# Optimization experiments

Hardware: AMD Instinct MI355X
Metric: run time of the kernel (lower is better)

## Reference

```python
import jax, jax.numpy as jnp
import numpy as np

B, SQ, SK, HID, H, D = 2, 2048, 2048, 1024, 16, 64
LN_EPS = 1e-12


def _sinusoid(seq_len):
    # [1,1,S,D]: first half sin, second half cos (RoFormer convention)
    pos = np.arange(seq_len, dtype=np.float32)[:, None]
    inv_freq = 1.0 / (10000.0 ** (np.arange(0, D, 2, dtype=np.float32) / D))
    ang = pos * inv_freq  # [S, D/2]
    return jnp.asarray(np.concatenate([np.sin(ang), np.cos(ang)], axis=-1)[None, None], dtype=jnp.float32)


def setup_inputs() -> dict:
    key = jax.random.key(0)
    ks = jax.random.split(key, 12)
    w = lambda k, shape: jax.random.normal(k, shape, dtype=jnp.float32) * 0.02
    return {
        "hidden_states": jax.random.normal(ks[0], (B, SQ, HID), dtype=jnp.float32),
        "encoder_hidden_states": jax.random.normal(ks[1], (B, SK, HID), dtype=jnp.float32),
        "encoder_attention_mask": jnp.zeros((B, 1, 1, SK), dtype=jnp.float32),  # additive mask
        "sinusoidal_pos": _sinusoid(SQ),
        "c_sinusoidal_pos": _sinusoid(SK),
        "Wq": w(ks[2], (HID, HID)), "bq": jnp.zeros((HID,), jnp.float32),
        "Wk": w(ks[3], (HID, HID)), "bk": jnp.zeros((HID,), jnp.float32),
        "Wv": w(ks[4], (HID, HID)), "bv": jnp.zeros((HID,), jnp.float32),
        "Wd": w(ks[5], (HID, HID)), "bd": jnp.zeros((HID,), jnp.float32),
        "ln_gamma": jnp.ones((HID,), jnp.float32),
        "ln_beta": jnp.zeros((HID,), jnp.float32),
    }


def apply_rope(sinusoidal_pos, layer):
    # sinusoidal_pos: [1,1,S,D] = sin||cos halves; layer: [B,H,S,D]
    sin, cos = jnp.split(sinusoidal_pos, 2, axis=-1)
    sin_pos = jnp.stack([sin, sin], axis=-1).reshape(sinusoidal_pos.shape)
    cos_pos = jnp.stack([cos, cos], axis=-1).reshape(sinusoidal_pos.shape)
    rot = jnp.stack([-layer[..., 1::2], layer[..., ::2]], axis=-1).reshape(layer.shape)
    return layer * cos_pos + rot * sin_pos


def _heads(x):
    b, s, _ = x.shape
    return x.reshape(b, s, H, D).transpose(0, 2, 1, 3)  # [B,H,S,D]


def reference(hidden_states, encoder_hidden_states, encoder_attention_mask,
              sinusoidal_pos, c_sinusoidal_pos,
              Wq, bq, Wk, bk, Wv, bv, Wd, bd, ln_gamma, ln_beta):
    q = _heads(hidden_states @ Wq.T + bq)
    k = _heads(encoder_hidden_states @ Wk.T + bk)
    v = _heads(encoder_hidden_states @ Wv.T + bv)
    q = apply_rope(sinusoidal_pos, q)
    k = apply_rope(c_sinusoidal_pos, k)

    scores = jnp.einsum("bhqd,bhkd->bhqk", q, k) / jnp.sqrt(jnp.float32(D))
    scores = scores + encoder_attention_mask  # broadcast [B,1,1,SK]
    probs = jax.nn.softmax(scores, axis=-1)
    ctx = jnp.einsum("bhqk,bhkd->bhqd", probs, v)
    ctx = ctx.transpose(0, 2, 1, 3).reshape(hidden_states.shape[0], -1, HID)

    proj = ctx @ Wd.T + bd
    x = hidden_states + proj
    mu = jnp.mean(x, axis=-1, keepdims=True)
    var = jnp.mean(jnp.square(x - mu), axis=-1, keepdims=True)
    return (x - mu) / jnp.sqrt(var + LN_EPS) * ln_gamma + ln_beta
```

## Files before the change

kernel.cpp:

```cpp
#include <hip/hip_runtime.h>

typedef __attribute__((ext_vector_type(8))) short short8;
typedef __attribute__((ext_vector_type(4))) float f32x4;
typedef __attribute__((ext_vector_type(16))) float f32x16;

#define LOG2E 1.4426950408889634f
#define QSCALE 0.18033688011112042f

#define ASM_VMCNT2() asm volatile("s_waitcnt vmcnt(2)" ::: "memory")
#define ASM_VMCNT1() asm volatile("s_waitcnt vmcnt(1)" ::: "memory")
#define ASM_VMCNT0() asm volatile("s_waitcnt vmcnt(0)" ::: "memory")
#define ASM_LGKM0()  asm volatile("s_waitcnt lgkmcnt(0)" ::: "memory")

static __device__ __forceinline__ unsigned short f2bf(float f){
  unsigned u = __builtin_bit_cast(unsigned, f);
  u += 0x7FFFu + ((u>>16)&1u);
  return (unsigned short)(u>>16);
}

static __device__ __forceinline__ void async16(const void* g, const void* l){
  __builtin_amdgcn_global_load_lds(
      (const __attribute__((address_space(1))) unsigned*)(unsigned long long)g,
      (__attribute__((address_space(3))) unsigned*)(unsigned)(unsigned long long)l,
      16, 0, 0);
}

__global__ __launch_bounds__(256) void prep_kernel(
    const float* __restrict__ hidden, unsigned short* __restrict__ hb,
    const float* __restrict__ encoder, unsigned short* __restrict__ eb,
    const float* __restrict__ Wq, unsigned short* __restrict__ wqb,
    const float* __restrict__ Wk, unsigned short* __restrict__ wkb,
    const float* __restrict__ Wv, unsigned short* __restrict__ wvb,
    const float* __restrict__ Wd, unsigned short* __restrict__ wdb,
    const float* __restrict__ mask, float* __restrict__ maskE)
{
  int blk = blockIdx.x;
  if (blk < 6144){
    const float* src; unsigned short* dst; int i;
    if (blk < 4096){
      int t = blk*256 + threadIdx.x;
      src = (t >> 19) ? encoder : hidden;
      dst = (t >> 19) ? eb : hb;
      i = (t & 524287)*8;
    } else {
      int t = (blk-4096)*256 + threadIdx.x;
      int z = t >> 17;
      src = (z==0)?Wq:(z==1)?Wk:(z==2)?Wv:Wd;
      dst = (z==0)?wqb:(z==1)?wkb:(z==2)?wvb:wdb;
      i = (t & 131071)*8;
    }
    const float4* s4 = (const float4*)(src + i);
    float4 a = s4[0], b = s4[1];
    union { unsigned short u[8]; short8 v; } o;
    o.u[0]=f2bf(a.x); o.u[1]=f2bf(a.y); o.u[2]=f2bf(a.z); o.u[3]=f2bf(a.w);
    o.u[4]=f2bf(b.x); o.u[5]=f2bf(b.y); o.u[6]=f2bf(b.z); o.u[7]=f2bf(b.w);
    *(short8*)(dst + i) = o.v;
  } else {
    int i = (blk-6144)*256 + threadIdx.x;
    float4 v = ((const float4*)mask)[i];
    v.x*=LOG2E; v.y*=LOG2E; v.z*=LOG2E; v.w*=LOG2E;
    ((float4*)maskE)[i] = v;
  }
}

__global__ __launch_bounds__(512) void gemm_qkv(
    const unsigned short* __restrict__ hb, const unsigned short* __restrict__ eb,
    const unsigned short* __restrict__ wqb, const unsigned short* __restrict__ wkb,
    const unsigned short* __restrict__ wvb,
    const float* __restrict__ bq, const float* __restrict__ bk, const float* __restrict__ bv,
    const float* __restrict__ sp, const float* __restrict__ csp,
    unsigned short* __restrict__ Qb, unsigned short* __restrict__ Kb, unsigned short* __restrict__ Vt)
{
  const int flat = blockIdx.x;
  const int work = (flat&7)*96 + (flat>>3);
  const int bn  = work & 7;
  const int zbm = work >> 3;
  const int z  = zbm >> 5;
  const int bm = zbm & 31;

  const unsigned short* A = (z==0) ? hb : eb;
  const unsigned short* W = (z==0) ? wqb : (z==1 ? wkb : wvb);
  const float* bias = (z==0) ? bq : (z==1 ? bk : bv);
  const float* rope = (z==0) ? sp : (z==1 ? csp : nullptr);

  __shared__ unsigned short As[3][128*32];
  __shared__ unsigned short Bs[3][128*32];

  const int tid = threadIdx.x;
  const int w = tid>>6, l = tid&63;
  const int wr = w>>1, wc = w&1;
  const int srow = tid>>2, scol = (tid&3)*8;

  const f32x4 zero = {0.f,0.f,0.f,0.f};
  f32x4 acc[2][4];
  #pragma unroll
  for (int mi=0;mi<2;mi++)
    #pragma unroll
    for (int ni=0;ni<4;ni++) acc[mi][ni] = zero;

  auto stage = [&](int buf, int kt){
    async16(A + (size_t)(bm*128 + srow)*1024 + kt*32 + scol, As[buf] + tid*8);
    async16(W + (size_t)(bn*128 + srow)*1024 + kt*32 + scol, Bs[buf] + tid*8);
  };

  stage(0, 0);

  int cur = 0;
  for (int kt=0; kt<32; ++kt){
    int nxt = (cur==2) ? 0 : cur+1;
    if (kt < 31){ stage(nxt, kt+1); ASM_VMCNT2(); }
    else        { ASM_VMCNT0(); }
    __builtin_amdgcn_s_barrier();
    __builtin_amdgcn_sched_barrier(0);

    short8 af[2], bf[4];
    #pragma unroll
    for (int mi=0;mi<2;mi++)
      af[mi] = *(const short8*)(As[cur] + (wr*32 + mi*16 + (l&15))*32 + (l>>4)*8);
    #pragma unroll
    for (int ni=0;ni<4;ni++)
      bf[ni] = *(const short8*)(Bs[cur] + (wc*64 + ni*16 + (l&15))*32 + (l>>4)*8);
    #pragma unroll
    for (int mi=0;mi<2;mi++)
      #pragma unroll
      for (int ni=0;ni<4;ni++)
        acc[mi][ni] = __builtin_amdgcn_mfma_f32_16x16x32_bf16(af[mi], bf[ni], acc[mi][ni], 0,0,0);

    cur = nxt;
  }

  if (z == 2){
    #pragma unroll
    for (int mi=0;mi<2;mi++){
      #pragma unroll
      for (int ni=0;ni<4;ni++){
        int mr0 = bm*128 + wr*32 + mi*16 + (l>>4)*4;
        int nc  = bn*128 + wc*64 + ni*16 + (l&15);
        int b0 = mr0>>11, s0 = mr0&2047;
        int h = nc>>6, d = nc&63;
        float bia = bias[nc];
        union { unsigned short u[4]; unsigned long long ull; } pk;
        #pragma unroll
        for (int r=0;r<4;r++) pk.u[r] = f2bf(acc[mi][ni][r] + bia);
        *(unsigned long long*)(Vt + ((size_t)(b0*16 + h)*64 + d)*2048 + s0) = pk.ull;
      }
    }
  } else {
    #pragma unroll
    for (int mi=0;mi<2;mi++){
      #pragma unroll
      for (int ni=0;ni<4;ni++){
        #pragma unroll
        for (int r=0;r<4;r++){
          int mr = bm*128 + wr*32 + mi*16 + (l>>4)*4 + r;
          int nc = bn*128 + wc*64 + ni*16 + (l&15);
          float v = acc[mi][ni][r] + bias[nc];
          int b = mr>>11, s = mr&2047;
          int h = nc>>6,  d = nc&63;
          float p = __shfl_xor(v, 1);
          float sv = rope[s*64 + (d>>1)];
          float cv = rope[s*64 + 32 + (d>>1)];
          float ov = (d&1) ? (v*cv + p*sv) : (v*cv - p*sv);
          if (z == 0) ov *= QSCALE;
          unsigned short* out = (z==0) ? Qb : Kb;
          out[((size_t)(b*16 + h)*2048 + s)*64 + d] = f2bf(ov);
        }
      }
    }
  }
}

__global__ __launch_bounds__(512) void flash_attn(
    const unsigned short* __restrict__ Qb, const unsigned short* __restrict__ Kb,
    const unsigned short* __restrict__ Vt, const float* __restrict__ maskE,
    unsigned short* __restrict__ ctx)
{
  __shared__ unsigned short Kls[2][2][4096];
  __shared__ unsigned short Vls[2][2][4096];
  __shared__ float maskLS[2048];

  const int tid = threadIdx.x;
  const int w = tid>>6, l = tid&63;
  const int qc = l&31, hi = l>>5;
  const int wq = w&3, half = w>>2;

  const int flat = blockIdx.x;
  const int o = (flat&7)*64 + (flat>>3);
  const int qt = o&15, bh = o>>4;
  const int b = bh>>4, h = bh&15;

  {
    ((float4*)maskLS)[tid] = ((const float4*)(maskE + b*2048))[tid];
  }

  const int qrow = qt*128 + wq*32 + qc;
  const unsigned short* qptr = Qb + ((size_t)bh*2048 + qrow)*64;
  short8 qf[4];
  #pragma unroll
  for (int ks=0;ks<4;ks++) qf[ks] = *(const short8*)(qptr + ks*16 + hi*8);

  float m_r = 0.f, l_r = 0.f;
  f32x16 oacc[2];
  #pragma unroll
  for (int t3=0;t3<2;t3++)
    #pragma unroll
    for (int i=0;i<16;i++) oacc[t3][i] = 0.f;

  const int srow = l>>3;
  const int scol = ((l&7) ^ srow)*8;
  const unsigned short* kSrc0; const unsigned short* kSrc1;
  const unsigned short* vSrc0; const unsigned short* vSrc1;
  {
    int c0 = wq*2, c1 = wq*2+1;
    kSrc0 = Kb + ((size_t)bh*2048 + half*1024 + c0*8 + srow)*64 + scol;
    kSrc1 = Kb + ((size_t)bh*2048 + half*1024 + c1*8 + srow)*64 + scol;
    vSrc0 = Vt + ((size_t)bh*64 + c0*8 + srow)*2048 + half*1024 + scol;
    vSrc1 = Vt + ((size_t)bh*64 + c1*8 + srow)*2048 + half*1024 + scol;
  }
  const int ld0 = (wq*2)*512 + l*8, ld1 = (wq*2+1)*512 + l*8;

  auto stage = [&](int buf){
    async16(kSrc0, &Kls[half][buf][ld0]);
    async16(kSrc1, &Kls[half][buf][ld1]);
    async16(vSrc0, &Vls[half][buf][ld0]);
    async16(vSrc1, &Vls[half][buf][ld1]);
    kSrc0 += 4096; kSrc1 += 4096;
    vSrc0 += 64;   vSrc1 += 64;
  };

  stage(0);
  __syncthreads();
  int cur = 0;

  const int rg0 = (qc&7);

  for (int ktl=0; ktl<16; ++ktl){
    if (ktl < 15) stage(cur^1);

    f32x16 sacc[2];
    #pragma unroll
    for (int t2=0;t2<2;t2++){
      #pragma unroll
      for (int rg=0;rg<4;rg++){
        const float4 mv = *(const float4*)&maskLS[half*1024 + ktl*64 + t2*32 + rg*8 + hi*4];
        sacc[t2][rg*4+0] = mv.x;
        sacc[t2][rg*4+1] = mv.y;
        sacc[t2][rg*4+2] = mv.z;
        sacc[t2][rg*4+3] = mv.w;
      }
    }

    __builtin_amdgcn_s_setprio(1);
    #pragma unroll
    for (int ks=0; ks<4; ++ks){
      const short8 kf0 = *(const short8*)(&Kls[half][cur][ qc*64      + (((ks*2+hi)^rg0)*8) ]);
      const short8 kf1 = *(const short8*)(&Kls[half][cur][ (32+qc)*64 + (((ks*2+hi)^rg0)*8) ]);
      sacc[0] = __builtin_amdgcn_mfma_f32_32x32x16_bf16(kf0, qf[ks], sacc[0], 0,0,0);
      sacc[1] = __builtin_amdgcn_mfma_f32_32x32x16_bf16(kf1, qf[ks], sacc[1], 0,0,0);
    }
    __builtin_amdgcn_s_setprio(0);

    float rs = 0.f;
    #pragma unroll
    for (int t2=0;t2<2;t2++)
      #pragma unroll
      for (int i=0;i<16;i++){
        float e = __builtin_amdgcn_exp2f(sacc[t2][i] - m_r);
        sacc[t2][i] = e;
        rs += e;
      }
    { float a = rs, c2 = rs;
      asm("v_permlane32_swap_b32 %0, %1" : "+v"(a), "+v"(c2));
      rs = a + c2; }

    if (__builtin_expect(!__all(rs <= 16777216.0f), 0)){
      float cm = 1.0f;
      #pragma unroll
      for (int t2=0;t2<2;t2++)
        #pragma unroll
        for (int i=0;i<16;i++) cm = fmaxf(cm, sacc[t2][i]);
      { float a = cm, c2 = cm;
        asm("v_permlane32_swap_b32 %0, %1" : "+v"(a), "+v"(c2));
        cm = fmaxf(a, c2); }
      float rin = 1.0f/cm;
      #pragma unroll
      for (int t2=0;t2<2;t2++)
        #pragma unroll
        for (int i=0;i<16;i++) sacc[t2][i] *= rin;
      #pragma unroll
      for (int t3=0;t3<2;t3++)
        #pragma unroll
        for (int i=0;i<16;i++) oacc[t3][i] *= rin;
      l_r *= rin;
      rs  *= rin;
      m_r += log2f(cm);
    }
    l_r += rs;

    short8 pB[4];
    #pragma unroll
    for (int t2=0;t2<2;t2++){
      #pragma unroll
      for (int hf=0; hf<2; ++hf){
        unsigned x0,x1,x2,x3;
        asm("v_cvt_pk_bf16_f32 %0, %1, %2" : "=v"(x0) : "v"(sacc[t2][hf*8+0]), "v"(sacc[t2][hf*8+1]));
        asm("v_cvt_pk_bf16_f32 %0, %1, %2" : "=v"(x1) : "v"(sacc[t2][hf*8+2]), "v"(sacc[t2][hf*8+3]));
        asm("v_cvt_pk_bf16_f32 %0, %1, %2" : "=v"(x2) : "v"(sacc[t2][hf*8+4]), "v"(sacc[t2][hf*8+5]));
        asm("v_cvt_pk_bf16_f32 %0, %1, %2" : "=v"(x3) : "v"(sacc[t2][hf*8+6]), "v"(sacc[t2][hf*8+7]));
        asm("v_permlane32_swap_b32 %0, %1" : "+v"(x2), "+v"(x0));
        asm("v_permlane32_swap_b32 %0, %1" : "+v"(x3), "+v"(x1));
        union { unsigned u[4]; short8 v; } pb;
        pb.u[0]=x0; pb.u[1]=x1; pb.u[2]=x2; pb.u[3]=x3;
        pB[t2*2+hf] = pb.v;
      }
    }

    __builtin_amdgcn_s_setprio(1);
    #pragma unroll
    for (int t3=0;t3<2;t3++){
      #pragma unroll
      for (int si=0; si<4; ++si){
        const short8 vf = *(const short8*)(&Vls[half][cur][ (t3*32+qc)*64 + (((si*2+hi)^rg0)*8) ]);
        oacc[t3] = __builtin_amdgcn_mfma_f32_32x32x16_bf16(vf, pB[si], oacc[t3], 0,0,0);
      }
    }
    __builtin_amdgcn_s_setprio(0);

    __syncthreads();
    cur ^= 1;
  }

  float* Ox  = (float*)&Kls[0][0][0];
  float* MLf = (float*)&Vls[0][0][0];

  if (half == 1){
    #pragma unroll
    for (int t3=0;t3<2;t3++){
      #pragma unroll
      for (int rg=0;rg<4;rg++){
        int dbase = t3*32 + rg*8 + hi*4;
        f32x4 o4 = { oacc[t3][rg*4+0], oacc[t3][rg*4+1], oacc[t3][rg*4+2], oacc[t3][rg*4+3] };
        *(f32x4*)&Ox[wq*2048 + qc*64 + (dbase ^ (rg0*8))] = o4;
      }
    }
    if (hi == 0){
      MLf[wq*64 + qc]      = m_r;
      MLf[wq*64 + 32 + qc] = l_r;
    }
  }
  __syncthreads();

  if (half == 0){
    float m1 = MLf[wq*64 + qc];
    float l1 = MLf[wq*64 + 32 + qc];
    float mstar = fmaxf(m_r, m1);
    float s0 = __builtin_amdgcn_exp2f(m_r - mstar);
    float s1 = __builtin_amdgcn_exp2f(m1 - mstar);
    float inv = 1.0f / (l_r*s0 + l1*s1);
    float a0 = s0*inv, a1 = s1*inv;

    int qglob = qt*128 + wq*32 + qc;
    unsigned short* cp = ctx + ((size_t)b*2048 + qglob)*1024 + h*64;
    #pragma unroll
    for (int t3=0;t3<2;t3++){
      #pragma unroll
      for (int rg=0;rg<4;rg++){
        int dbase = t3*32 + rg*8 + hi*4;
        f32x4 o1 = *(const f32x4*)&Ox[wq*2048 + qc*64 + (dbase ^ (rg0*8))];
        union { unsigned short u[4]; unsigned long long ull; } pk4;
        #pragma unroll
        for (int i=0;i<4;i++) pk4.u[i] = f2bf(oacc[t3][rg*4+i]*a0 + o1[i]*a1);
        *(unsigned long long*)(cp + dbase) = pk4.ull;
      }
    }
  }
}

__global__ __launch_bounds__(512) void gemm_proj(
    const unsigned short* __restrict__ ctxb, const unsigned short* __restrict__ wdb,
    const float* __restrict__ bd, const float* __restrict__ hidden,
    float* __restrict__ X)
{
  const int flat = blockIdx.x;
  const int work = (flat&7)*64 + (flat>>3);
  const int bn = work & 7;
  const int bm = work >> 3;

  __shared__ unsigned short As[3][64*32];
  __shared__ unsigned short Bs[3][128*32];
  const int tid = threadIdx.x;
  const int w = tid>>6, l = tid&63;
  const int wr = w>>2, wc = w&3;

  const f32x4 zero = {0.f,0.f,0.f,0.f};
  f32x4 acc[2][2];
  #pragma unroll
  for (int mi=0;mi<2;mi++)
    #pragma unroll
    for (int ni=0;ni<2;ni++) acc[mi][ni] = zero;

  auto stage = [&](int buf, int kt){
    if (tid < 256)
      async16(ctxb + (size_t)(bm*64 + (tid>>2))*1024 + kt*32 + (tid&3)*8, As[buf] + tid*8);
    async16(wdb + (size_t)(bn*128 + (tid>>2))*1024 + kt*32 + (tid&3)*8, Bs[buf] + tid*8);
  };

  stage(0, 0);

  int cur = 0;
  for (int kt=0; kt<32; ++kt){
    int nxt = (cur==2) ? 0 : cur+1;
    if (kt < 31){
      stage(nxt, kt+1);
      if (w < 4) ASM_VMCNT2(); else ASM_VMCNT1();
    } else {
      ASM_VMCNT0();
    }
    __builtin_amdgcn_s_barrier();
    __builtin_amdgcn_sched_barrier(0);

    short8 af[2], bf[2];
    #pragma unroll
    for (int mi=0;mi<2;mi++)
      af[mi] = *(const short8*)(As[cur] + (wr*32 + mi*16 + (l&15))*32 + (l>>4)*8);
    #pragma unroll
    for (int ni=0;ni<2;ni++)
      bf[ni] = *(const short8*)(Bs[cur] + (wc*32 + ni*16 + (l&15))*32 + (l>>4)*8);
    #pragma unroll
    for (int mi=0;mi<2;mi++)
      #pragma unroll
      for (int ni=0;ni<2;ni++)
        acc[mi][ni] = __builtin_amdgcn_mfma_f32_16x16x32_bf16(af[mi], bf[ni], acc[mi][ni], 0,0,0);

    cur = nxt;
  }

  #pragma unroll
  for (int mi=0;mi<2;mi++){
    #pragma unroll
    for (int ni=0;ni<2;ni++){
      #pragma unroll
      for (int r=0;r<4;r++){
        int mr = bm*64 + wr*32 + mi*16 + (l>>4)*4 + r;
        int nc = bn*128 + wc*32 + ni*16 + (l&15);
        float v = acc[mi][ni][r] + bd[nc] + hidden[(size_t)mr*1024 + nc];
        X[(size_t)mr*1024 + nc] = v;
      }
    }
  }
}

__global__ __launch_bounds__(256) void ln_kernel(
    const float* __restrict__ X, const float* __restrict__ gamma,
    const float* __restrict__ beta, float* __restrict__ out)
{
  const int row = blockIdx.x;
  const int tid = threadIdx.x;
  const float4 v = ((const float4*)(X + (size_t)row*1024))[tid];
  float s  = v.x+v.y+v.z+v.w;
  float ss = v.x*v.x + v.y*v.y + v.z*v.z + v.w*v.w;
  #pragma unroll
  for (int off=1; off<64; off<<=1){
    s  += __shfl_xor(s, off);
    ss += __shfl_xor(ss, off);
  }
  __shared__ float red[8];
  const int w = tid>>6, l = tid&63;
  if (l == 0){ red[w] = s; red[4+w] = ss; }
  __syncthreads();
  s  = red[0]+red[1]+red[2]+red[3];
  ss = red[4]+red[5]+red[6]+red[7];
  float mu  = s*(1.f/1024.f);
  float var = ss*(1.f/1024.f) - mu*mu;
  float inv = rsqrtf(var + 1e-12f);
  const float4 g  = ((const float4*)gamma)[tid];
  const float4 bt = ((const float4*)beta)[tid];
  float4 o;
  o.x = (v.x-mu)*inv*g.x + bt.x;
  o.y = (v.y-mu)*inv*g.y + bt.y;
  o.z = (v.z-mu)*inv*g.z + bt.z;
  o.w = (v.w-mu)*inv*g.w + bt.w;
  ((float4*)(out + (size_t)row*1024))[tid] = o;
}

extern "C" void kernel_launch(void* const* d_in, const int* in_sizes, int n_in,
                              void* d_out, int out_size, void* d_ws, size_t ws_size,
                              hipStream_t stream) {
  const float* hidden  = (const float*)d_in[0];
  const float* encoder = (const float*)d_in[1];
  const float* mask    = (const float*)d_in[2];
  const float* sp      = (const float*)d_in[3];
  const float* csp     = (const float*)d_in[4];
  const float* Wq = (const float*)d_in[5];  const float* bq = (const float*)d_in[6];
  const float* Wk = (const float*)d_in[7];  const float* bk = (const float*)d_in[8];
  const float* Wv = (const float*)d_in[9];  const float* bv = (const float*)d_in[10];
  const float* Wd = (const float*)d_in[11]; const float* bd = (const float*)d_in[12];
  const float* gamma = (const float*)d_in[13];
  const float* beta  = (const float*)d_in[14];

  char* ws = (char*)d_ws;
  const size_t MB_ = 1ull<<20;
  unsigned short* hb  = (unsigned short*)(ws + 0);
  unsigned short* eb  = (unsigned short*)(ws + 8*MB_);
  unsigned short* wqb = (unsigned short*)(ws + 16*MB_);
  unsigned short* wkb = (unsigned short*)(ws + 18*MB_);
  unsigned short* wvb = (unsigned short*)(ws + 20*MB_);
  unsigned short* wdb = (unsigned short*)(ws + 22*MB_);
  unsigned short* Qb  = (unsigned short*)(ws + 24*MB_);
  unsigned short* Kb  = (unsigned short*)(ws + 32*MB_);
  unsigned short* Vt  = (unsigned short*)(ws + 40*MB_);
  unsigned short* ctxb = hb;
  float* X = (float*)(ws + 24*MB_);
  float* maskE = (float*)(ws + 48*MB_);

  prep_kernel<<<6148,256,0,stream>>>(hidden, hb, encoder, eb,
                                     Wq, wqb, Wk, wkb, Wv, wvb, Wd, wdb,
                                     mask, maskE);

  gemm_qkv<<<768,512,0,stream>>>(hb, eb, wqb, wkb, wvb,
                                 bq, bk, bv, sp, csp, Qb, Kb, Vt);
  flash_attn<<<512,512,0,stream>>>(Qb, Kb, Vt, maskE, ctxb);
  gemm_proj<<<512,512,0,stream>>>(ctxb, wdb, bd, hidden, X);
  ln_kernel<<<4096,256,0,stream>>>(X, gamma, beta, (float*)d_out);
}
```

Before: 121.8 us.

## Split keys four ways in flash attention, store residual in bf16

```diff
diff --git a/kernel.cpp b/kernel.cpp
--- a/kernel.cpp
+++ b/kernel.cpp
@@ -16,6 +16,9 @@
   unsigned u = __builtin_bit_cast(unsigned, f);
   u += 0x7FFFu + ((u>>16)&1u);
   return (unsigned short)(u>>16);
+}
+static __device__ __forceinline__ float bf2f(unsigned short u){
+  return __builtin_bit_cast(float, ((unsigned)u)<<16);
 }
 
 static __device__ __forceinline__ void async16(const void* g, const void* l){
@@ -170,30 +173,29 @@
   }
 }
 
-__global__ __launch_bounds__(512) void flash_attn(
+__global__ __launch_bounds__(512, 8) void flash_attn(
     const unsigned short* __restrict__ Qb, const unsigned short* __restrict__ Kb,
     const unsigned short* __restrict__ Vt, const float* __restrict__ maskE,
     unsigned short* __restrict__ ctx)
 {
-  __shared__ unsigned short Kls[2][2][4096];
-  __shared__ unsigned short Vls[2][2][4096];
-  __shared__ float maskLS[2048];
+  __shared__ char LDSm[40960];
+  unsigned short* Kls = (unsigned short*)LDSm;
+  unsigned short* Vls = (unsigned short*)(LDSm + 16384);
+  float* maskLS = (float*)(LDSm + 32768);
 
   const int tid = threadIdx.x;
   const int w = tid>>6, l = tid&63;
   const int qc = l&31, hi = l>>5;
-  const int wq = w&3, half = w>>2;
+  const int wq = w&1, qr = w>>1;
 
   const int flat = blockIdx.x;
-  const int o = (flat&7)*64 + (flat>>3);
-  const int qt = o&15, bh = o>>4;
+  const int o = (flat&7)*128 + (flat>>3);
+  const int qt2 = o&31, bh = o>>5;
   const int b = bh>>4, h = bh&15;
 
-  {
-    ((float4*)maskLS)[tid] = ((const float4*)(maskE + b*2048))[tid];
-  }
-
-  const int qrow = qt*128 + wq*32 + qc;
+  ((float4*)maskLS)[tid] = ((const float4*)(maskE + b*2048))[tid];
+
+  const int qrow = qt2*64 + wq*32 + qc;
   const unsigned short* qptr = Qb + ((size_t)bh*2048 + qrow)*64;
   short8 qf[4];
   #pragma unroll
@@ -206,87 +208,76 @@
     #pragma unroll
     for (int i=0;i<16;i++) oacc[t3][i] = 0.f;
 
-  const int srow = l>>3;
-  const int scol = ((l&7) ^ srow)*8;
-  const unsigned short* kSrc0; const unsigned short* kSrc1;
-  const unsigned short* vSrc0; const unsigned short* vSrc1;
-  {
-    int c0 = wq*2, c1 = wq*2+1;
-    kSrc0 = Kb + ((size_t)bh*2048 + half*1024 + c0*8 + srow)*64 + scol;
-    kSrc1 = Kb + ((size_t)bh*2048 + half*1024 + c1*8 + srow)*64 + scol;
-    vSrc0 = Vt + ((size_t)bh*64 + c0*8 + srow)*2048 + half*1024 + scol;
-    vSrc1 = Vt + ((size_t)bh*64 + c1*8 + srow)*2048 + half*1024 + scol;
-  }
-  const int ld0 = (wq*2)*512 + l*8, ld1 = (wq*2+1)*512 + l*8;
-
-  auto stage = [&](int buf){
-    async16(kSrc0, &Kls[half][buf][ld0]);
-    async16(kSrc1, &Kls[half][buf][ld1]);
-    async16(vSrc0, &Vls[half][buf][ld0]);
-    async16(vSrc1, &Vls[half][buf][ld1]);
-    kSrc0 += 4096; kSrc1 += 4096;
-    vSrc0 += 64;   vSrc1 += 64;
-  };
-
-  stage(0);
-  __syncthreads();
-  int cur = 0;
-
-  const int rg0 = (qc&7);
-
-  for (int ktl=0; ktl<16; ++ktl){
-    if (ktl < 15) stage(cur^1);
-
-    f32x16 sacc[2];
-    #pragma unroll
-    for (int t2=0;t2<2;t2++){
-      #pragma unroll
-      for (int rg=0;rg<4;rg++){
-        const float4 mv = *(const float4*)&maskLS[half*1024 + ktl*64 + t2*32 + rg*8 + hi*4];
-        sacc[t2][rg*4+0] = mv.x;
-        sacc[t2][rg*4+1] = mv.y;
-        sacc[t2][rg*4+2] = mv.z;
-        sacc[t2][rg*4+3] = mv.w;
-      }
-    }
-
+  const int u = tid & 127;
+  const int uj1 = u + 128;
+  const int kr0 = u>>3,   kg0 = u&7;
+  const int kr1 = uj1>>3, kg1 = uj1&7;
+  const int vr0 = u>>2,   vg0 = u&3;
+  const int vr1 = uj1>>2, vg1 = uj1&3;
+  const unsigned short* kS0 = Kb + ((size_t)bh*2048 + qr*512 + kr0)*64 + ((kg0 ^ (kr0&7))*8);
+  const unsigned short* kS1 = Kb + ((size_t)bh*2048 + qr*512 + kr1)*64 + ((kg1 ^ (kr1&7))*8);
+  const unsigned short* vS0 = Vt + ((size_t)bh*64 + vr0)*2048 + qr*512 + ((vg0 ^ (vr0&3))*8);
+  const unsigned short* vS1 = Vt + ((size_t)bh*64 + vr1)*2048 + qr*512 + ((vg1 ^ (vr1&3))*8);
+  unsigned short* kD0 = Kls + qr*2048 + u*8;
+  unsigned short* kD1 = Kls + qr*2048 + uj1*8;
+  unsigned short* vD0 = Vls + qr*2048 + u*8;
+  unsigned short* vD1 = Vls + qr*2048 + uj1*8;
+
+  async16(kS0, kD0); async16(kS1, kD1);
+  kS0 += 2048; kS1 += 2048;
+  ASM_LGKM0();
+
+  const int rg0q = qc&7;
+
+  for (int t=0; t<16; ++t){
+    __builtin_amdgcn_s_barrier();
+    async16(vS0, vD0); async16(vS1, vD1);
+    vS0 += 32; vS1 += 32;
+    ASM_VMCNT2();
+    __builtin_amdgcn_sched_barrier(0);
+
+    f32x16 sacc;
+    #pragma unroll
+    for (int rg=0;rg<4;rg++){
+      const float4 mv = *(const float4*)&maskLS[qr*512 + t*32 + rg*8 + hi*4];
+      sacc[rg*4+0] = mv.x; sacc[rg*4+1] = mv.y;
+      sacc[rg*4+2] = mv.z; sacc[rg*4+3] = mv.w;
+    }
     __builtin_amdgcn_s_setprio(1);
     #pragma unroll
     for (int ks=0; ks<4; ++ks){
-      const short8 kf0 = *(const short8*)(&Kls[half][cur][ qc*64      + (((ks*2+hi)^rg0)*8) ]);
-      const short8 kf1 = *(const short8*)(&Kls[half][cur][ (32+qc)*64 + (((ks*2+hi)^rg0)*8) ]);
-      sacc[0] = __builtin_amdgcn_mfma_f32_32x32x16_bf16(kf0, qf[ks], sacc[0], 0,0,0);
-      sacc[1] = __builtin_amdgcn_mfma_f32_32x32x16_bf16(kf1, qf[ks], sacc[1], 0,0,0);
+      const short8 kf = *(const short8*)(Kls + qr*2048 + qc*64 + (((ks*2+hi) ^ rg0q)*8));
+      sacc = __builtin_amdgcn_mfma_f32_32x32x16_bf16(kf, qf[ks], sacc, 0,0,0);
     }
     __builtin_amdgcn_s_setprio(0);
 
+    ASM_LGKM0();
+    __builtin_amdgcn_s_barrier();
+    if (t < 15){
+      async16(kS0, kD0); async16(kS1, kD1);
+      kS0 += 2048; kS1 += 2048;
+    }
+
     float rs = 0.f;
     #pragma unroll
-    for (int t2=0;t2<2;t2++)
-      #pragma unroll
-      for (int i=0;i<16;i++){
-        float e = __builtin_amdgcn_exp2f(sacc[t2][i] - m_r);
-        sacc[t2][i] = e;
-        rs += e;
-      }
+    for (int i=0;i<16;i++){
+      float e = __builtin_amdgcn_exp2f(sacc[i] - m_r);
+      sacc[i] = e;
+      rs += e;
+    }
     { float a = rs, c2 = rs;
       asm("v_permlane32_swap_b32 %0, %1" : "+v"(a), "+v"(c2));
       rs = a + c2; }
-
     if (__builtin_expect(!__all(rs <= 16777216.0f), 0)){
       float cm = 1.0f;
       #pragma unroll
-      for (int t2=0;t2<2;t2++)
-        #pragma unroll
-        for (int i=0;i<16;i++) cm = fmaxf(cm, sacc[t2][i]);
+      for (int i=0;i<16;i++) cm = fmaxf(cm, sacc[i]);
       { float a = cm, c2 = cm;
         asm("v_permlane32_swap_b32 %0, %1" : "+v"(a), "+v"(c2));
         cm = fmaxf(a, c2); }
       float rin = 1.0f/cm;
       #pragma unroll
-      for (int t2=0;t2<2;t2++)
-        #pragma unroll
-        for (int i=0;i<16;i++) sacc[t2][i] *= rin;
+      for (int i=0;i<16;i++) sacc[i] *= rin;
       #pragma unroll
       for (int t3=0;t3<2;t3++)
         #pragma unroll
@@ -297,50 +288,87 @@
     }
     l_r += rs;
 
-    short8 pB[4];
-    #pragma unroll
-    for (int t2=0;t2<2;t2++){
-      #pragma unroll
-      for (int hf=0; hf<2; ++hf){
-        unsigned x0,x1,x2,x3;
-        asm("v_cvt_pk_bf16_f32 %0, %1, %2" : "=v"(x0) : "v"(sacc[t2][hf*8+0]), "v"(sacc[t2][hf*8+1]));
-        asm("v_cvt_pk_bf16_f32 %0, %1, %2" : "=v"(x1) : "v"(sacc[t2][hf*8+2]), "v"(sacc[t2][hf*8+3]));
-        asm("v_cvt_pk_bf16_f32 %0, %1, %2" : "=v"(x2) : "v"(sacc[t2][hf*8+4]), "v"(sacc[t2][hf*8+5]));
-        asm("v_cvt_pk_bf16_f32 %0, %1, %2" : "=v"(x3) : "v"(sacc[t2][hf*8+6]), "v"(sacc[t2][hf*8+7]));
-        asm("v_permlane32_swap_b32 %0, %1" : "+v"(x2), "+v"(x0));
-        asm("v_permlane32_swap_b32 %0, %1" : "+v"(x3), "+v"(x1));
-        union { unsigned u[4]; short8 v; } pb;
-        pb.u[0]=x0; pb.u[1]=x1; pb.u[2]=x2; pb.u[3]=x3;
-        pB[t2*2+hf] = pb.v;
-      }
-    }
+    short8 pB[2];
+    #pragma unroll
+    for (int hf=0; hf<2; ++hf){
+      unsigned x0,x1,x2,x3;
+      asm("v_cvt_pk_bf16_f32 %0, %1, %2" : "=v"(x0) : "v"(sacc[hf*8+0]), "v"(sacc[hf*8+1]));
+      asm("v_cvt_pk_bf16_f32 %0, %1, %2" : "=v"(x1) : "v"(sacc[hf*8+2]), "v"(sacc[hf*8+3]));
+      asm("v_cvt_pk_bf16_f32 %0, %1, %2" : "=v"(x2) : "v"(sacc[hf*8+4]), "v"(sacc[hf*8+5]));
+      asm("v_cvt_pk_bf16_f32 %0, %1, %2" : "=v"(x3) : "v"(sacc[hf*8+6]), "v"(sacc[hf*8+7]));
+      asm("v_permlane32_swap_b32 %0, %1" : "+v"(x2), "+v"(x0));
+      asm("v_permlane32_swap_b32 %0, %1" : "+v"(x3), "+v"(x1));
+      union { unsigned uu[4]; short8 v; } pb;
+      pb.uu[0]=x0; pb.uu[1]=x1; pb.uu[2]=x2; pb.uu[3]=x3;
+      pB[hf] = pb.v;
+    }
+
+    if (t < 15) ASM_VMCNT2(); else ASM_VMCNT0();
+    __builtin_amdgcn_sched_barrier(0);
 
     __builtin_amdgcn_s_setprio(1);
     #pragma unroll
     for (int t3=0;t3<2;t3++){
       #pragma unroll
-      for (int si=0; si<4; ++si){
-        const short8 vf = *(const short8*)(&Vls[half][cur][ (t3*32+qc)*64 + (((si*2+hi)^rg0)*8) ]);
+      for (int si=0; si<2; ++si){
+        const short8 vf = *(const short8*)(Vls + qr*2048 + (t3*32+qc)*32 + (((si*2+hi) ^ (qc&3))*8));
         oacc[t3] = __builtin_amdgcn_mfma_f32_32x32x16_bf16(vf, pB[si], oacc[t3], 0,0,0);
       }
     }
     __builtin_amdgcn_s_setprio(0);
-
-    __syncthreads();
-    cur ^= 1;
-  }
-
-  float* Ox  = (float*)&Kls[0][0][0];
-  float* MLf = (float*)&Vls[0][0][0];
-
-  if (half == 1){
+    ASM_LGKM0();
+  }
+  __syncthreads();
+
+  float* Ox  = (float*)LDSm;
+  float* MLf = maskLS;
+
+  if (qr & 1){
+    int reg = wq*2 + (qr>>1);
     #pragma unroll
     for (int t3=0;t3<2;t3++){
       #pragma unroll
       for (int rg=0;rg<4;rg++){
         int dbase = t3*32 + rg*8 + hi*4;
         f32x4 o4 = { oacc[t3][rg*4+0], oacc[t3][rg*4+1], oacc[t3][rg*4+2], oacc[t3][rg*4+3] };
-        *(f32x4*)&Ox[wq*2048 + qc*64 + (dbase ^ (rg0*8))] = o4;
+        *(f32x4*)&Ox[reg*2048 + qc*64 + (dbase ^ (rg0q*8))] = o4;
+      }
+    }
+    if (hi == 0){
+      MLf[((qr>>1)*2 + wq)*64 + qc]      = m_r;
+      MLf[((qr>>1)*2 + wq)*64 + 32 + qc] = l_r;
+    }
+  }
+  __syncthreads();
+  if (!(qr & 1)){
+    int reg = wq*2 + (qr>>1);
+    float m1 = MLf[((qr>>1)*2 + wq)*64 + qc];
+    float l1 = MLf[((qr>>1)*2 + wq)*64 + 32 + qc];
+    float mstar = fmaxf(m_r, m1);
+    float s0 = __builtin_amdgcn_exp2f(m_r - mstar);
+    float s1 = __builtin_amdgcn_exp2f(m1 - mstar);
+    l_r = l_r*s0 + l1*s1;
+    m_r = mstar;
+    #pragma unroll
+    for (int t3=0;t3<2;t3++){
+      #pragma unroll
+      for (int rg=0;rg<4;rg++){
+        int dbase = t3*32 + rg*8 + hi*4;
+        f32x4 o1 = *(const f32x4*)&Ox[reg*2048 + qc*64 + (dbase ^ (rg0q*8))];
+        #pragma unroll
+        for (int i=0;i<4;i++) oacc[t3][rg*4+i] = oacc[t3][rg*4+i]*s0 + o1[i]*s1;
+      }
+    }
+  }
+  __syncthreads();
+  if (qr == 2){
+    #pragma unroll
+    for (int t3=0;t3<2;t3++){
+      #pragma unroll
+      for (int rg=0;rg<4;rg++){
+        int dbase = t3*32 + rg*8 + hi*4;
+        f32x4 o4 = { oacc[t3][rg*4+0], oacc[t3][rg*4+1], oacc[t3][rg*4+2], oacc[t3][rg*4+3] };
+        *(f32x4*)&Ox[wq*2048 + qc*64 + (dbase ^ (rg0q*8))] = o4;
       }
     }
     if (hi == 0){
@@ -349,8 +377,7 @@
     }
   }
   __syncthreads();
-
-  if (half == 0){
+  if (qr == 0){
     float m1 = MLf[wq*64 + qc];
     float l1 = MLf[wq*64 + 32 + qc];
     float mstar = fmaxf(m_r, m1);
@@ -359,17 +386,17 @@
     float inv = 1.0f / (l_r*s0 + l1*s1);
     float a0 = s0*inv, a1 = s1*inv;
 
-    int qglob = qt*128 + wq*32 + qc;
+    int qglob = qt2*64 + wq*32 + qc;
     unsigned short* cp = ctx + ((size_t)b*2048 + qglob)*1024 + h*64;
     #pragma unroll
     for (int t3=0;t3<2;t3++){
       #pragma unroll
       for (int rg=0;rg<4;rg++){
         int dbase = t3*32 + rg*8 + hi*4;
-        f32x4 o1 = *(const f32x4*)&Ox[wq*2048 + qc*64 + (dbase ^ (rg0*8))];
-        union { unsigned short u[4]; unsigned long long ull; } pk4;
+        f32x4 o1 = *(const f32x4*)&Ox[wq*2048 + qc*64 + (dbase ^ (rg0q*8))];
+        union { unsigned short uu[4]; unsigned long long ull; } pk4;
         #pragma unroll
-        for (int i=0;i<4;i++) pk4.u[i] = f2bf(oacc[t3][rg*4+i]*a0 + o1[i]*a1);
+        for (int i=0;i<4;i++) pk4.uu[i] = f2bf(oacc[t3][rg*4+i]*a0 + o1[i]*a1);
         *(unsigned long long*)(cp + dbase) = pk4.ull;
       }
     }
@@ -378,8 +405,8 @@
 
 __global__ __launch_bounds__(512) void gemm_proj(
     const unsigned short* __restrict__ ctxb, const unsigned short* __restrict__ wdb,
-    const float* __restrict__ bd, const float* __restrict__ hidden,
-    float* __restrict__ X)
+    const float* __restrict__ bd, const unsigned short* __restrict__ hb,
+    unsigned short* __restrict__ X)
 {
   const int flat = blockIdx.x;
   const int work = (flat&7)*64 + (flat>>3);
@@ -443,22 +470,26 @@
       for (int r=0;r<4;r++){
         int mr = bm*64 + wr*32 + mi*16 + (l>>4)*4 + r;
         int nc = bn*128 + wc*32 + ni*16 + (l&15);
-        float v = acc[mi][ni][r] + bd[nc] + hidden[(size_t)mr*1024 + nc];
-        X[(size_t)mr*1024 + nc] = v;
+        float v = acc[mi][ni][r] + bd[nc] + bf2f(hb[(size_t)mr*1024 + nc]);
+        X[(size_t)mr*1024 + nc] = f2bf(v);
       }
     }
   }
 }
 
 __global__ __launch_bounds__(256) void ln_kernel(
-    const float* __restrict__ X, const float* __restrict__ gamma,
+    const unsigned short* __restrict__ X, const float* __restrict__ gamma,
     const float* __restrict__ beta, float* __restrict__ out)
 {
   const int row = blockIdx.x;
   const int tid = threadIdx.x;
-  const float4 v = ((const float4*)(X + (size_t)row*1024))[tid];
-  float s  = v.x+v.y+v.z+v.w;
-  float ss = v.x*v.x + v.y*v.y + v.z*v.z + v.w*v.w;
+  uint2 raw = ((const uint2*)(X + (size_t)row*1024))[tid];
+  float v0 = __builtin_bit_cast(float, (raw.x & 0xFFFFu) << 16);
+  float v1 = __builtin_bit_cast(float, raw.x & 0xFFFF0000u);
+  float v2 = __builtin_bit_cast(float, (raw.y & 0xFFFFu) << 16);
+  float v3 = __builtin_bit_cast(float, raw.y & 0xFFFF0000u);
+  float s  = v0+v1+v2+v3;
+  float ss = v0*v0 + v1*v1 + v2*v2 + v3*v3;
   #pragma unroll
   for (int off=1; off<64; off<<=1){
     s  += __shfl_xor(s, off);
@@ -475,12 +506,12 @@
   float inv = rsqrtf(var + 1e-12f);
   const float4 g  = ((const float4*)gamma)[tid];
   const float4 bt = ((const float4*)beta)[tid];
-  float4 o;
-  o.x = (v.x-mu)*inv*g.x + bt.x;
-  o.y = (v.y-mu)*inv*g.y + bt.y;
-  o.z = (v.z-mu)*inv*g.z + bt.z;
-  o.w = (v.w-mu)*inv*g.w + bt.w;
-  ((float4*)(out + (size_t)row*1024))[tid] = o;
+  float4 oo;
+  oo.x = (v0-mu)*inv*g.x + bt.x;
+  oo.y = (v1-mu)*inv*g.y + bt.y;
+  oo.z = (v2-mu)*inv*g.z + bt.z;
+  oo.w = (v3-mu)*inv*g.w + bt.w;
+  ((float4*)(out + (size_t)row*1024))[tid] = oo;
 }
 
 extern "C" void kernel_launch(void* const* d_in, const int* in_sizes, int n_in,
@@ -509,8 +540,8 @@
   unsigned short* Qb  = (unsigned short*)(ws + 24*MB_);
   unsigned short* Kb  = (unsigned short*)(ws + 32*MB_);
   unsigned short* Vt  = (unsigned short*)(ws + 40*MB_);
-  unsigned short* ctxb = hb;
-  float* X = (float*)(ws + 24*MB_);
+  unsigned short* ctxb = eb;
+  unsigned short* X = Qb;
   float* maskE = (float*)(ws + 48*MB_);
 
   prep_kernel<<<6148,256,0,stream>>>(hidden, hb, encoder, eb,
@@ -519,7 +550,7 @@
 
   gemm_qkv<<<768,512,0,stream>>>(hb, eb, wqb, wkb, wvb,
                                  bq, bk, bv, sp, csp, Qb, Kb, Vt);
-  flash_attn<<<512,512,0,stream>>>(Qb, Kb, Vt, maskE, ctxb);
-  gemm_proj<<<512,512,0,stream>>>(ctxb, wdb, bd, hidden, X);
+  flash_attn<<<1024,512,0,stream>>>(Qb, Kb, Vt, maskE, ctxb);
+  gemm_proj<<<512,512,0,stream>>>(ctxb, wdb, bd, hb, X);
   ln_kernel<<<4096,256,0,stream>>>(X, gamma, beta, (float*)d_out);
 }
```

After: 360.2 us. 2.96x slower.
